# Optimization experiments

Hardware: AMD Instinct MI355X
Metric: run time of the kernel (lower is better)

## Reference

```python
import jax, jax.numpy as jnp
import numpy as np

K = 256          # num_embeddings
D = 128          # embedding_dim
COMMIT = 0.25
DECAY = 0.99
EPS = 1e-5


def setup_inputs() -> dict:
    key = jax.random.key(0)
    k1, k2, k3 = jax.random.split(key, 3)
    z = jax.random.normal(k1, (128, D, 32, 32), dtype=jnp.float32)
    codebook = jax.random.uniform(k2, (K, D), dtype=jnp.float32, minval=-1.0 / K, maxval=1.0 / K)
    ema_count = jnp.ones((K,), dtype=jnp.float32)
    ema_weight = jax.random.normal(k3, (K, D), dtype=jnp.float32)
    return {"z": z, "codebook": codebook, "ema_count": ema_count, "ema_weight": ema_weight}


def reference(z, codebook, ema_count, ema_weight):
    B, C, H, W = z.shape
    # [B,C,H,W] -> [B*H*W, C]
    z_flat = z.transpose(0, 2, 3, 1).reshape(-1, C)
    N = z_flat.shape[0]

    # squared L2 distances to codebook: [N, K]
    d = (z_flat * z_flat).sum(1, keepdims=True) \
        - 2.0 * (z_flat @ codebook.T) \
        + (codebook * codebook).sum(1)
    idx = jnp.argmin(d, axis=1)                      # [N]

    # codebook lookup (equivalent to one-hot @ codebook, without materializing one-hot)
    quantized_flat = codebook[idx]                   # [N, D]
    quantized = quantized_flat.reshape(B, H, W, C).transpose(0, 3, 1, 2)

    # EMA codebook update (training branch; random unused-entry reset omitted)
    ones = jnp.ones((N,), dtype=z_flat.dtype)
    enc_sum = jax.ops.segment_sum(ones, idx, num_segments=K)          # [K]
    enc_batch = jax.ops.segment_sum(z_flat, idx, num_segments=K)      # [K, D]
    new_count = DECAY * ema_count + (1.0 - DECAY) * enc_sum
    new_weight = DECAY * ema_weight + (1.0 - DECAY) * enc_batch
    n = new_count.sum()
    normalized_count = (new_count + EPS) / (n + K * EPS) * n
    new_codebook = new_weight / normalized_count[:, None]

    # losses
    codebook_loss = jnp.mean((jax.lax.stop_gradient(z) - quantized) ** 2)
    commitment_loss = COMMIT * jnp.mean((jax.lax.stop_gradient(quantized) - z) ** 2)

    # straight-through estimator
    quantized_st = z + jax.lax.stop_gradient(quantized - z)

    return (quantized_st, idx.reshape(B, H, W), commitment_loss, codebook_loss,
            new_codebook, new_count, new_weight)
```

## Files before the change

### kernel.cpp

```cpp
#include <hip/hip_runtime.h>

#define K 256
#define D 128
#define HW 1024
#define CHW 131072
#define N_TOT 131072
#define NELEM 16777216

#define WS_C2 0
#define WS_ENCSUM 256
#define WS_ENCB 512
#define WS_LOSS 33280
#define WS_FLAGCNT 33281
#define WS_LIST 33282
#define FLAG_CAP 16384
#define WS_PART 49666
#define PBLK 64
#define PSTRIDE 33024
#define WS_CBT (WS_PART + PBLK * PSTRIDE)
#define WS_CBH 2195972
#define WS_CBL 2212356

#define OUT_Q 0
#define OUT_IDX 16777216
#define OUT_COMMIT 16908288
#define OUT_CBLOSS 16908289
#define OUT_NEWCB 16908290
#define OUT_NEWCNT 16941058
#define OUT_NEWW 16941314

#define TAU 5e-5f
#define MT 64
#define ZST 68

typedef __attribute__((ext_vector_type(8))) short short8;
typedef __attribute__((ext_vector_type(4))) float floatx4;

__device__ __forceinline__ void cvt_split(const float* xv, short8* hi, short8* lo) {
    union U { uint32_t u[4]; short8 s; } H, L;
    #pragma unroll
    for (int p = 0; p < 4; ++p) {
        uint32_t u0 = __float_as_uint(xv[2 * p]);
        uint32_t u1 = __float_as_uint(xv[2 * p + 1]);
        H.u[p] = (u0 >> 16) | (u1 & 0xFFFF0000u);
        float h0 = __uint_as_float(u0 & 0xFFFF0000u);
        float h1 = __uint_as_float(u1 & 0xFFFF0000u);
        float l0 = xv[2 * p] - h0;
        float l1 = xv[2 * p + 1] - h1;
        L.u[p] = (__float_as_uint(l0) >> 16) | (__float_as_uint(l1) & 0xFFFF0000u);
    }
    *hi = H.s; *lo = L.s;
}

__global__ void k_prep(const float* __restrict__ cb, float* __restrict__ ws) {
    #pragma clang fp contract(off)
    const int blk = blockIdx.x, t = threadIdx.x;
    if (blk == 0) {
        int k = t;
        if (k == 0) { ws[WS_LOSS] = 0.0f; ((int*)ws)[WS_FLAGCNT] = 0; }
        const float* row = cb + (size_t)k * D;
        float r[8];
        #pragma unroll
        for (int j = 0; j < 8; ++j) r[j] = row[j] * row[j];
        for (int i = 8; i < D; i += 8) {
            #pragma unroll
            for (int j = 0; j < 8; ++j) r[j] = r[j] + row[i + j] * row[i + j];
        }
        ws[WS_C2 + k] = ((r[0] + r[1]) + (r[2] + r[3])) + ((r[4] + r[5]) + (r[6] + r[7]));
    } else {
        int e = (blk - 1) * 4 + (t >> 6);
        int lane = t & 63;
        int ds = e >> 4, ktg = e & 15;
        int code = ktg * 16 + (lane & 15);
        int d0 = ds * 32 + (lane >> 4) * 8;
        float xv[8];
        #pragma unroll
        for (int j = 0; j < 8; ++j) xv[j] = cb[(size_t)code * D + d0 + j];
        short8 h, l;
        cvt_split(xv, &h, &l);
        union V { short8 s; uint4 u; } Hv, Lv;
        Hv.s = h; Lv.s = l;
        uint32_t* wsu = (uint32_t*)ws;
        reinterpret_cast<uint4*>(wsu + WS_CBH)[e * 64 + lane] = Hv.u;
        reinterpret_cast<uint4*>(wsu + WS_CBL)[e * 64 + lane] = Lv.u;
    }
}

__global__ void __launch_bounds__(256, 4)
k_main(const float* __restrict__ z, const float* __restrict__ cb,
       float* __restrict__ ws, float* __restrict__ out) {
    __shared__ float zs[D * ZST];
    __shared__ float c2L[K];
    __shared__ float mgB[2][MT];
    __shared__ float mgS[2][MT];
    __shared__ int   mgK[2][MT];
    __shared__ int bkA[MT];
    __shared__ float lsw[4];

    const int t = threadIdx.x;
    const int blk = blockIdx.x;
    const int n0 = blk * MT;
    const int b = n0 >> 10;
    const int hw0 = n0 & 1023;

    c2L[t] = -0.5f * ws[WS_C2 + t];

    {
        const float4* __restrict__ z4 = reinterpret_cast<const float4*>(z);
        const size_t zbase4 = (size_t)b * (CHW / 4) + (hw0 >> 2);
        #pragma unroll
        for (int i = 0; i < 8; ++i) {
            int f = i * 256 + t;
            int dd = f >> 4, n4 = f & 15;
            float4 v = z4[zbase4 + (size_t)dd * (HW / 4) + n4];
            *reinterpret_cast<float4*>(&zs[dd * ZST + 4 * n4]) = v;
        }
    }
    __syncthreads();

    const int lane = t & 63, w = t >> 6;
    const int col = lane & 15, quad = lane >> 4;
    const int kh = w & 1;
    const int mh = w >> 1;

    short8 Ah[2][4], Al[2][4];
    {
        const int rbase = quad * 8 * ZST + mh * 32 + col;
        #pragma unroll
        for (int mt = 0; mt < 2; ++mt)
            #pragma unroll
            for (int ds = 0; ds < 4; ++ds) {
                float xv[8];
                #pragma unroll
                for (int j = 0; j < 8; ++j)
                    xv[j] = zs[rbase + (ds * 32 + j) * ZST + mt * 16];
                cvt_split(xv, &Ah[mt][ds], &Al[mt][ds]);
            }
    }

    const uint32_t* wsu = (const uint32_t*)ws;
    const uint4* __restrict__ bh4 = reinterpret_cast<const uint4*>(wsu + WS_CBH);
    const uint4* __restrict__ bl4 = reinterpret_cast<const uint4*>(wsu + WS_CBL);

    float best[2][4], second[2][4];
    int bk[2][4];
    #pragma unroll
    for (int mt = 0; mt < 2; ++mt)
        #pragma unroll
        for (int r = 0; r < 4; ++r) { best[mt][r] = -3.4e38f; second[mt][r] = -3.4e38f; bk[mt][r] = 0; }

    #pragma unroll
    for (int kt = 0; kt < 8; ++kt) {
        float iv = c2L[kh * 128 + kt * 16 + col];
        floatx4 acc[2];
        #pragma unroll
        for (int mt = 0; mt < 2; ++mt) {
            acc[mt][0] = iv; acc[mt][1] = iv; acc[mt][2] = iv; acc[mt][3] = iv;
        }
        union V { uint4 u; short8 s; } BX[4], BY[4];
        #pragma unroll
        for (int ds = 0; ds < 4; ++ds) {
            int fi = (ds * 16 + kh * 8 + kt) * 64 + lane;
            BX[ds].u = bh4[fi];
            BY[ds].u = bl4[fi];
        }
        #pragma unroll
        for (int ds = 0; ds < 4; ++ds) {
            #pragma unroll
            for (int mt = 0; mt < 2; ++mt) {
                acc[mt] = __builtin_amdgcn_mfma_f32_16x16x32_bf16(Ah[mt][ds], BX[ds].s, acc[mt], 0, 0, 0);
                acc[mt] = __builtin_amdgcn_mfma_f32_16x16x32_bf16(Ah[mt][ds], BY[ds].s, acc[mt], 0, 0, 0);
                acc[mt] = __builtin_amdgcn_mfma_f32_16x16x32_bf16(Al[mt][ds], BX[ds].s, acc[mt], 0, 0, 0);
            }
        }
        int kc = kh * 128 + kt * 16 + col;
        #pragma unroll
        for (int mt = 0; mt < 2; ++mt)
            #pragma unroll
            for (int r = 0; r < 4; ++r) {
                float s = acc[mt][r];
                if (s > best[mt][r]) { second[mt][r] = best[mt][r]; best[mt][r] = s; bk[mt][r] = kc; }
                else if (s > second[mt][r]) second[mt][r] = s;
            }
    }

    #pragma unroll
    for (int off = 1; off < 16; off <<= 1) {
        #pragma unroll
        for (int mt = 0; mt < 2; ++mt)
            #pragma unroll
            for (int r = 0; r < 4; ++r) {
                float ob = __shfl_xor(best[mt][r], off);
                float os = __shfl_xor(second[mt][r], off);
                int ok = __shfl_xor(bk[mt][r], off);
                float nb = fmaxf(best[mt][r], ob);
                float ns = fmaxf(fminf(best[mt][r], ob), fmaxf(second[mt][r], os));
                bk[mt][r] = (ob > best[mt][r]) ? ok : bk[mt][r];
                best[mt][r] = nb; second[mt][r] = ns;
            }
    }

    if (col == 0) {
        #pragma unroll
        for (int mt = 0; mt < 2; ++mt)
            #pragma unroll
            for (int r = 0; r < 4; ++r) {
                int nl = mh * 32 + mt * 16 + quad * 4 + r;
                mgB[kh][nl] = best[mt][r];
                mgS[kh][nl] = second[mt][r];
                mgK[kh][nl] = bk[mt][r];
            }
    }
    __syncthreads();

    if (t < MT) {
        float B1 = mgB[0][t], S = mgS[0][t];
        int KB = mgK[0][t];
        {
            float ob = mgB[1][t], os = mgS[1][t];
            int ok = mgK[1][t];
            float nb = fmaxf(B1, ob);
            float ns = fmaxf(fminf(B1, ob), fmaxf(S, os));
            KB = (ob > B1) ? ok : KB;
            B1 = nb; S = ns;
        }
        int n = n0 + t;
        bool fl = (B1 - S) < TAU;
        if (fl) {
            int slot = atomicAdd((int*)ws + WS_FLAGCNT, 1);
            if (slot < FLAG_CAP) ((int*)ws)[WS_LIST + slot] = n;
            else fl = false;
        }
        if (!fl) { out[OUT_IDX + n] = (float)KB; bkA[t] = KB; }
        else bkA[t] = -1;
    }
    __syncthreads();

    const int nl = t & 63, dp = t >> 6;
    const int bkn = bkA[nl];
    float lsum = 0.0f;
    if (bkn >= 0) {
        const float4* __restrict__ cb4 = reinterpret_cast<const float4*>(cb);
        float* __restrict__ op = out + OUT_Q + (size_t)b * CHW + hw0 + nl;
        #pragma unroll
        for (int u = 0; u < 8; ++u) {
            float4 q4 = cb4[bkn * 32 + dp * 8 + u];
            int d = dp * 32 + u * 4;
            #pragma unroll
            for (int cc = 0; cc < 4; ++cc) {
                float zv = zs[(d + cc) * ZST + nl];
                float q = ((const float*)&q4)[cc];
                op[(size_t)(d + cc) * HW] = zv + (q - zv);
                float tdf = zv - q;
                lsum = fmaf(tdf, tdf, lsum);
            }
        }
    }
    #pragma unroll
    for (int off = 32; off >= 1; off >>= 1) lsum += __shfl_down(lsum, off);
    if ((t & 63) == 0) lsw[w] = lsum;
    __syncthreads();
    if (t == 0) atomicAdd(ws + WS_LOSS, (lsw[0] + lsw[1]) + (lsw[2] + lsw[3]));
}

__global__ void k_fallback(const float* __restrict__ z, const float* __restrict__ cb,
                           float* __restrict__ ws, float* __restrict__ out) {
    #pragma clang fp contract(off)
    const int tid = threadIdx.x;
    __shared__ float zsF[D];
    __shared__ float z2s;
    __shared__ float dvals[K];
    __shared__ int kidx[K];

    int cnt = ((const int*)ws)[WS_FLAGCNT];
    if (cnt > FLAG_CAP) cnt = FLAG_CAP;

    for (int li = blockIdx.x; li < cnt; li += gridDim.x) {
        const int n = ((const int*)ws)[WS_LIST + li];
        const int b = n >> 10;
        const int hw = n & 1023;

        if (tid < D) zsF[tid] = z[(size_t)b * CHW + (size_t)tid * HW + hw];
        __syncthreads();

        if (tid == 0) {
            float r[8];
            #pragma unroll
            for (int j = 0; j < 8; ++j) r[j] = zsF[j] * zsF[j];
            for (int i = 8; i < D; i += 8) {
                #pragma unroll
                for (int j = 0; j < 8; ++j) r[j] = r[j] + zsF[i + j] * zsF[i + j];
            }
            z2s = ((r[0] + r[1]) + (r[2] + r[3])) + ((r[4] + r[5]) + (r[6] + r[7]));
        }
        __syncthreads();

        {
            const float4* __restrict__ row4 =
                reinterpret_cast<const float4*>(cb + (size_t)tid * D);
            double a0 = 0.0, a1 = 0.0, a2 = 0.0, a3 = 0.0;
            #pragma unroll 4
            for (int d4 = 0; d4 < 32; ++d4) {
                float4 cv = row4[d4];
                const float* zz = &zsF[d4 * 4];
                a0 += (double)zz[0] * (double)cv.x;
                a1 += (double)zz[1] * (double)cv.y;
                a2 += (double)zz[2] * (double)cv.z;
                a3 += (double)zz[3] * (double)cv.w;
            }
            float zc = (float)((a0 + a1) + (a2 + a3));
            float dq = (z2s - 2.0f * zc) + ws[WS_C2 + tid];
            dvals[tid] = dq;
            kidx[tid] = tid;
        }
        __syncthreads();

        for (int s = K / 2; s > 0; s >>= 1) {
            if (tid < s) {
                float ov = dvals[tid + s]; int ok = kidx[tid + s];
                float mv = dvals[tid];     int mk2 = kidx[tid];
                if (ov < mv || (ov == mv && ok < mk2)) { dvals[tid] = ov; kidx[tid] = ok; }
            }
            __syncthreads();
        }
        const int bk = kidx[0];
        __syncthreads();

        float t2 = 0.0f;
        if (tid == 0) out[OUT_IDX + n] = (float)bk;
        if (tid < D) {
            float q = cb[(size_t)bk * D + tid];
            out[OUT_Q + (size_t)b * CHW + (size_t)tid * HW + hw] = zsF[tid] + (q - zsF[tid]);
            float t = zsF[tid] - q;
            t2 = t * t;
        }
        dvals[tid] = t2;
        __syncthreads();
        for (int s = K / 2; s > 0; s >>= 1) {
            if (tid < s) dvals[tid] += dvals[tid + s];
            __syncthreads();
        }
        if (tid == 0) atomicAdd(ws + WS_LOSS, dvals[0]);
        __syncthreads();
    }
}

#define GN 2048
__global__ void k_sort(const float* __restrict__ out, float* __restrict__ ws) {
    __shared__ int idxs[GN];
    __shared__ int cnt[K];
    __shared__ int incl[K];
    __shared__ int fill[K];

    const int t = threadIdx.x;
    const int p = blockIdx.x;

    if (t < K) cnt[t] = 0;
    __syncthreads();
    for (int j = t; j < GN; j += 1024) {
        int k = (int)out[OUT_IDX + (size_t)p * GN + j];
        idxs[j] = k;
        atomicAdd(&cnt[k], 1);
    }
    __syncthreads();
    if (t < K) incl[t] = cnt[t];
    __syncthreads();
    for (int off = 1; off < K; off <<= 1) {
        int v = 0;
        if (t < K) { v = incl[t]; if (t >= off) v += incl[t - off]; }
        __syncthreads();
        if (t < K) incl[t] = v;
        __syncthreads();
    }
    if (t < K) {
        const int st = incl[t] - cnt[t];
        fill[t] = st;
        ((int*)ws)[WS_LIST + p * K + t] = (st << 16) | cnt[t];
        ws[WS_PART + (size_t)p * PSTRIDE + K * D + t] = (float)cnt[t];
    }
    __syncthreads();

    unsigned short* ord = (unsigned short*)(ws + WS_CBT);
    for (int j = t; j < GN; j += 1024) {
        int k = idxs[j];
        int pos = atomicAdd(&fill[k], 1);
        ord[p * GN + pos] = (unsigned short)j;
    }
}

#define GZST 2052
__global__ void __launch_bounds__(1024, 4)
k_gather(const float* __restrict__ z, float* __restrict__ ws) {
    __shared__ float zsg[8 * GZST];
    __shared__ unsigned short ords[GN];
    __shared__ int skc[K];

    const int t = threadIdx.x;
    const int p = blockIdx.x >> 4;
    const int c = blockIdx.x & 15;

    const unsigned short* ord = (const unsigned short*)(ws + WS_CBT);
    for (int j = t; j < GN; j += 1024) ords[j] = ord[p * GN + j];
    if (t < K) skc[t] = ((const int*)ws)[WS_LIST + p * K + t];

    const float4* __restrict__ z4 = reinterpret_cast<const float4*>(z);
    for (int j = t; j < 8 * 512; j += 1024) {
        int d2 = j >> 9, n4 = j & 511;
        int bb = n4 >> 8, hw4 = n4 & 255;
        float4 v = z4[(size_t)(2 * p + bb) * (CHW / 4)
                      + (size_t)(c * 8 + d2) * (HW / 4) + hw4];
        *reinterpret_cast<float4*>(&zsg[d2 * GZST + 4 * n4]) = v;
    }
    __syncthreads();

    const int dl = t & 7;
    const int k0 = (t >> 3) * 2;
    float* __restrict__ pout = ws + WS_PART + (size_t)p * PSTRIDE;
    const float* __restrict__ zrow = zsg + dl * GZST;
    #pragma unroll
    for (int kk = 0; kk < 2; ++kk) {
        int k = k0 + kk;
        int sc = skc[k];
        int s = sc >> 16, e = s + (sc & 0xFFFF);
        float a = 0.0f;
        for (int q = s; q < e; ++q) a += zrow[ords[q]];
        pout[(size_t)k * D + c * 8 + dl] = a;
    }
}

__global__ void k_finalize(const float* __restrict__ ema_count,
                           const float* __restrict__ ema_weight,
                           const float* __restrict__ ws, float* __restrict__ out) {
    #pragma clang fp contract(off)
    const int tid = threadIdx.x;
    const int blk = blockIdx.x;
    __shared__ float red[K];
    __shared__ float normc[K];

    const float DEC = 0.99f;
    const float OMD = (float)(1.0 - 0.99);

    float es = 0.0f;
    {
        const float* __restrict__ ps = ws + WS_PART + K * D + tid;
        #pragma unroll 8
        for (int g = 0; g < PBLK; ++g) es += ps[(size_t)g * PSTRIDE];
    }
    float nc = DEC * ema_count[tid] + OMD * es;
    red[tid] = nc;
    __syncthreads();
    for (int s = K / 2; s > 0; s >>= 1) {
        if (tid < s) red[tid] += red[tid + s];
        __syncthreads();
    }
    const float nt = red[0];
    normc[tid] = (nc + 1e-5f) / (nt + 0.00256f) * nt;
    __syncthreads();

    if (blk == 0) {
        out[OUT_NEWCNT + tid] = nc;
        if (tid == 0) {
            float m = ws[WS_LOSS] / 16777216.0f;
            out[OUT_CBLOSS] = m;
            out[OUT_COMMIT] = 0.25f * m;
        }
    }

    const int i = blk * 256 + tid;
    float eb = 0.0f;
    {
        const float* __restrict__ pb = ws + WS_PART + i;
        #pragma unroll 8
        for (int g = 0; g < PBLK; ++g) eb += pb[(size_t)g * PSTRIDE];
    }
    const int k = i >> 7;
    float nw = DEC * ema_weight[i] + OMD * eb;
    out[OUT_NEWW + i] = nw;
    out[OUT_NEWCB + i] = nw / normc[k];
}

extern "C" void kernel_launch(void* const* d_in, const int* in_sizes, int n_in,
                              void* d_out, int out_size, void* d_ws, size_t ws_size,
                              hipStream_t stream) {
    const float* z = (const float*)d_in[0];
    const float* cb = (const float*)d_in[1];
    const float* ema_count = (const float*)d_in[2];
    const float* ema_weight = (const float*)d_in[3];
    float* out = (float*)d_out;
    float* ws = (float*)d_ws;

    k_prep<<<17, 256, 0, stream>>>(cb, ws);
    k_main<<<N_TOT / MT, 256, 0, stream>>>(z, cb, ws, out);
    k_fallback<<<4096, 256, 0, stream>>>(z, cb, ws, out);
    k_sort<<<64, 1024, 0, stream>>>(out, ws);
    k_gather<<<1024, 1024, 0, stream>>>(z, ws);
    k_finalize<<<128, 256, 0, stream>>>(ema_count, ema_weight, ws, out);
}
```

Measured before the change: 227.3 us.

## Fuse sort and gather into one LDS-atomic segment-sum kernel, split MFMA accumulators

The separate sort and gather kernels are replaced by one kernel. Each block loads z tiles into LDS transposed and accumulates per-code sums with shared-memory atomics, which removes one launch and the global ordering buffer. In the main distance kernel the three bf16-split MFMA products now go into separate accumulators, which breaks the serial dependency chain and may change rounding slightly. Occupancy is lowered to make room for the extra registers. The LDS float atomics may contend and make the summation order nondeterministic.

```diff
diff --git a/kernel.cpp b/kernel.cpp
--- a/kernel.cpp
+++ b/kernel.cpp
@@ -86,7 +86,7 @@
     }
 }
 
-__global__ void __launch_bounds__(256, 4)
+__global__ void __launch_bounds__(256, 3)
 k_main(const float* __restrict__ z, const float* __restrict__ cb,
        float* __restrict__ ws, float* __restrict__ out) {
     __shared__ float zs[D * ZST];
@@ -152,10 +152,12 @@
     #pragma unroll
     for (int kt = 0; kt < 8; ++kt) {
         float iv = c2L[kh * 128 + kt * 16 + col];
-        floatx4 acc[2];
+        floatx4 aH[2], aM[2], aL[2];
         #pragma unroll
         for (int mt = 0; mt < 2; ++mt) {
-            acc[mt][0] = iv; acc[mt][1] = iv; acc[mt][2] = iv; acc[mt][3] = iv;
+            aH[mt][0] = iv; aH[mt][1] = iv; aH[mt][2] = iv; aH[mt][3] = iv;
+            aM[mt][0] = 0.0f; aM[mt][1] = 0.0f; aM[mt][2] = 0.0f; aM[mt][3] = 0.0f;
+            aL[mt][0] = 0.0f; aL[mt][1] = 0.0f; aL[mt][2] = 0.0f; aL[mt][3] = 0.0f;
         }
         union V { uint4 u; short8 s; } BX[4], BY[4];
         #pragma unroll
@@ -168,9 +170,9 @@
         for (int ds = 0; ds < 4; ++ds) {
             #pragma unroll
             for (int mt = 0; mt < 2; ++mt) {
-                acc[mt] = __builtin_amdgcn_mfma_f32_16x16x32_bf16(Ah[mt][ds], BX[ds].s, acc[mt], 0, 0, 0);
-                acc[mt] = __builtin_amdgcn_mfma_f32_16x16x32_bf16(Ah[mt][ds], BY[ds].s, acc[mt], 0, 0, 0);
-                acc[mt] = __builtin_amdgcn_mfma_f32_16x16x32_bf16(Al[mt][ds], BX[ds].s, acc[mt], 0, 0, 0);
+                aH[mt] = __builtin_amdgcn_mfma_f32_16x16x32_bf16(Ah[mt][ds], BX[ds].s, aH[mt], 0, 0, 0);
+                aM[mt] = __builtin_amdgcn_mfma_f32_16x16x32_bf16(Ah[mt][ds], BY[ds].s, aM[mt], 0, 0, 0);
+                aL[mt] = __builtin_amdgcn_mfma_f32_16x16x32_bf16(Al[mt][ds], BX[ds].s, aL[mt], 0, 0, 0);
             }
         }
         int kc = kh * 128 + kt * 16 + col;
@@ -178,7 +180,7 @@
         for (int mt = 0; mt < 2; ++mt)
             #pragma unroll
             for (int r = 0; r < 4; ++r) {
-                float s = acc[mt][r];
+                float s = (aH[mt][r] + aM[mt][r]) + aL[mt][r];
                 if (s > best[mt][r]) { second[mt][r] = best[mt][r]; best[mt][r] = s; bk[mt][r] = kc; }
                 else if (s > second[mt][r]) second[mt][r] = s;
             }
@@ -346,86 +348,65 @@
 }
 
 #define GN 2048
-__global__ void k_sort(const float* __restrict__ out, float* __restrict__ ws) {
-    __shared__ int idxs[GN];
-    __shared__ int cnt[K];
-    __shared__ int incl[K];
-    __shared__ int fill[K];
+__global__ void __launch_bounds__(1024, 1)
+k_gather(const float* __restrict__ z, const float* __restrict__ out,
+         float* __restrict__ ws) {
+    __shared__ float acc[K * 32];
+    __shared__ float zst[128 * 33];
+    __shared__ int ks[GN];
+    __shared__ int cntL[K];
 
     const int t = threadIdx.x;
-    const int p = blockIdx.x;
-
-    if (t < K) cnt[t] = 0;
-    __syncthreads();
-    for (int j = t; j < GN; j += 1024) {
-        int k = (int)out[OUT_IDX + (size_t)p * GN + j];
-        idxs[j] = k;
-        atomicAdd(&cnt[k], 1);
-    }
-    __syncthreads();
-    if (t < K) incl[t] = cnt[t];
-    __syncthreads();
-    for (int off = 1; off < K; off <<= 1) {
-        int v = 0;
-        if (t < K) { v = incl[t]; if (t >= off) v += incl[t - off]; }
-        __syncthreads();
-        if (t < K) incl[t] = v;
-        __syncthreads();
-    }
-    if (t < K) {
-        const int st = incl[t] - cnt[t];
-        fill[t] = st;
-        ((int*)ws)[WS_LIST + p * K + t] = (st << 16) | cnt[t];
-        ws[WS_PART + (size_t)p * PSTRIDE + K * D + t] = (float)cnt[t];
-    }
-    __syncthreads();
-
-    unsigned short* ord = (unsigned short*)(ws + WS_CBT);
-    for (int j = t; j < GN; j += 1024) {
-        int k = idxs[j];
-        int pos = atomicAdd(&fill[k], 1);
-        ord[p * GN + pos] = (unsigned short)j;
-    }
-}
-
-#define GZST 2052
-__global__ void __launch_bounds__(1024, 4)
-k_gather(const float* __restrict__ z, float* __restrict__ ws) {
-    __shared__ float zsg[8 * GZST];
-    __shared__ unsigned short ords[GN];
-    __shared__ int skc[K];
-
-    const int t = threadIdx.x;
-    const int p = blockIdx.x >> 4;
-    const int c = blockIdx.x & 15;
-
-    const unsigned short* ord = (const unsigned short*)(ws + WS_CBT);
-    for (int j = t; j < GN; j += 1024) ords[j] = ord[p * GN + j];
-    if (t < K) skc[t] = ((const int*)ws)[WS_LIST + p * K + t];
+    const int p = blockIdx.x >> 2;
+    const int dh = blockIdx.x & 3;
+
+    #pragma unroll
+    for (int i = 0; i < 8; ++i) acc[i * 1024 + t] = 0.0f;
+    if (t < K) cntL[t] = 0;
+    for (int j = t; j < GN; j += 1024)
+        ks[j] = (int)out[OUT_IDX + (size_t)p * GN + j];
+    __syncthreads();
+    if (dh == 0) {
+        for (int j = t; j < GN; j += 1024) atomicAdd(&cntL[ks[j]], 1);
+    }
 
     const float4* __restrict__ z4 = reinterpret_cast<const float4*>(z);
-    for (int j = t; j < 8 * 512; j += 1024) {
-        int d2 = j >> 9, n4 = j & 511;
-        int bb = n4 >> 8, hw4 = n4 & 255;
-        float4 v = z4[(size_t)(2 * p + bb) * (CHW / 4)
-                      + (size_t)(c * 8 + d2) * (HW / 4) + hw4];
-        *reinterpret_cast<float4*>(&zsg[d2 * GZST + 4 * n4]) = v;
-    }
-    __syncthreads();
-
-    const int dl = t & 7;
-    const int k0 = (t >> 3) * 2;
+    const int d2s = t >> 5;
+    const int hl = t & 31;
+    const int d2a = t & 31;
+    const int ng = t >> 5;
+
+    float4 v = z4[(size_t)(2 * p) * (CHW / 4)
+                  + (size_t)(dh * 32 + d2s) * (HW / 4) + hl];
+    #pragma unroll 1
+    for (int r = 0; r < 16; ++r) {
+        #pragma unroll
+        for (int c = 0; c < 4; ++c)
+            zst[(hl * 4 + c) * 33 + d2s] = ((const float*)&v)[c];
+        __syncthreads();
+        if (r < 15) {
+            int n0r = (r + 1) * 128;
+            int bb = n0r >> 10, hwb = n0r & 1023;
+            v = z4[(size_t)(2 * p + bb) * (CHW / 4)
+                   + (size_t)(dh * 32 + d2s) * (HW / 4) + (hwb >> 2) + hl];
+        }
+        #pragma unroll
+        for (int i = 0; i < 4; ++i) {
+            int nl = ng * 4 + i;
+            int k = ks[r * 128 + nl];
+            atomicAdd(&acc[k * 32 + d2a], zst[nl * 33 + d2a]);
+        }
+        __syncthreads();
+    }
+
     float* __restrict__ pout = ws + WS_PART + (size_t)p * PSTRIDE;
-    const float* __restrict__ zrow = zsg + dl * GZST;
-    #pragma unroll
-    for (int kk = 0; kk < 2; ++kk) {
-        int k = k0 + kk;
-        int sc = skc[k];
-        int s = sc >> 16, e = s + (sc & 0xFFFF);
-        float a = 0.0f;
-        for (int q = s; q < e; ++q) a += zrow[ords[q]];
-        pout[(size_t)k * D + c * 8 + dl] = a;
-    }
+    #pragma unroll
+    for (int it = 0; it < 8; ++it) {
+        int idx = it * 1024 + t;
+        int k = idx >> 5, d2 = idx & 31;
+        pout[(size_t)k * D + dh * 32 + d2] = acc[idx];
+    }
+    if (dh == 0 && t < K) pout[K * D + t] = (float)cntL[t];
 }
 
 __global__ void k_finalize(const float* __restrict__ ema_count,
@@ -492,7 +473,6 @@
     k_prep<<<17, 256, 0, stream>>>(cb, ws);
     k_main<<<N_TOT / MT, 256, 0, stream>>>(z, cb, ws, out);
     k_fallback<<<4096, 256, 0, stream>>>(z, cb, ws, out);
-    k_sort<<<64, 1024, 0, stream>>>(out, ws);
-    k_gather<<<1024, 1024, 0, stream>>>(z, ws);
+    k_gather<<<256, 1024, 0, stream>>>(z, out, ws);
     k_finalize<<<128, 256, 0, stream>>>(ema_count, ema_weight, ws, out);
 }
```

Measured after the change: 298.4 us. +31.3%, slower.
